# Optimization experiments

Measured on AMD Instinct MI355X. Metric: run time of the kernel, lower is better.

Reference implementation:

```python
import jax, jax.numpy as jnp
import numpy as np

DIM = 1024
DIM_HEAD = 64
HEADS = 16
DIM_INNER = DIM_HEAD * HEADS  # 1024


def setup_inputs() -> dict:
    key = jax.random.key(0)
    k1, k2, k3 = jax.random.split(key, 3)
    b, n = 2, 2048
    x = jax.random.normal(k1, (b, n, DIM), dtype=jnp.float32)
    gamma = jnp.ones((DIM,), dtype=jnp.float32)
    # torch Linear weight [out,in] applied as x @ W.T; store pre-transposed [in,out]
    w_qkv = jax.random.normal(k2, (DIM, 3 * DIM_INNER), dtype=jnp.float32) * (DIM ** -0.5)
    w_out = jax.random.normal(k3, (DIM_INNER, DIM), dtype=jnp.float32) * (DIM_INNER ** -0.5)
    return {"x": x, "gamma": gamma, "w_qkv": w_qkv, "w_out": w_out}


def reference(x, gamma, w_qkv, w_out):
    h, d = HEADS, DIM_HEAD
    scale = d ** -0.5
    rms_scale = DIM ** 0.5
    # RMSNorm: F.normalize(x, dim=-1) * sqrt(dim) * gamma  (eps=1e-12 clamp on L2 norm)
    norm = jnp.maximum(jnp.linalg.norm(x, axis=-1, keepdims=True), 1e-12)
    xn = x / norm * rms_scale * gamma
    b, n, _ = x.shape
    qkv = xn @ w_qkv  # [b, n, 3*h*d]
    qkv = qkv.reshape(b, n, 3, h, d)
    q = qkv[:, :, 0].transpose(0, 2, 1, 3) * scale  # [b, h, n, d]
    k = qkv[:, :, 1].transpose(0, 2, 1, 3)
    v = qkv[:, :, 2].transpose(0, 2, 1, 3)
    sim = jnp.einsum('bhid,bhjd->bhij', q, k)  # [b, h, n, n]
    causal_mask = jnp.triu(jnp.ones((n, n), dtype=bool), k=1)
    neg = -jnp.finfo(sim.dtype).max
    sim = jnp.where(causal_mask, neg, sim)
    attn = jax.nn.softmax(sim, axis=-1)
    out = jnp.einsum('bhij,bhjd->bhid', attn, v)  # [b, h, n, d]
    out = out.transpose(0, 2, 1, 3).reshape(b, n, h * d)
    return out @ w_out
```

## Files before the change

### kernel.cpp

```cpp
#include <hip/hip_runtime.h>
#include <hip/hip_bf16.h>

typedef __bf16 bf16x8 __attribute__((ext_vector_type(8)));
typedef short s16x4 __attribute__((ext_vector_type(4)));
typedef float f32x4 __attribute__((ext_vector_type(4)));
typedef unsigned short u16x8 __attribute__((ext_vector_type(8)));

#define MFMA_K32(a, b, c) __builtin_amdgcn_mfma_f32_16x16x32_bf16(a, b, c, 0, 0, 0)

static __device__ __forceinline__ f32x4 mfma_k16(s16x4 a, s16x4 b, f32x4 c) {
#ifdef __HIP_DEVICE_COMPILE__
    return __builtin_amdgcn_mfma_f32_16x16x16bf16_1k(a, b, c, 0, 0, 0);
#else
    return c;
#endif
}

static __device__ __forceinline__ float fast_exp2(float x) {
#ifdef __HIP_DEVICE_COMPILE__
    return __builtin_amdgcn_exp2f(x);
#else
    return x;
#endif
}

#define GLL16(gp, lp)                                              \
    __builtin_amdgcn_global_load_lds(                              \
        (const __attribute__((address_space(1))) void*)(gp),       \
        (__attribute__((address_space(3))) void*)(lp), 16, 0, 0)

static __device__ __forceinline__ unsigned short f2bf(float f) {
    unsigned int u = __float_as_uint(f);
    u += 0x7fffu + ((u >> 16) & 1u);
    return (unsigned short)(u >> 16);
}

static __device__ __forceinline__ unsigned int cvtpk_bf16(float lo, float hi) {
#if defined(__HIP_DEVICE_COMPILE__) && __has_builtin(__builtin_amdgcn_cvt_pk_bf16_f32)
    typedef __bf16 bf16x2 __attribute__((ext_vector_type(2)));
    bf16x2 r = __builtin_amdgcn_cvt_pk_bf16_f32(lo, hi);
    return __builtin_bit_cast(unsigned int, r);
#else
    return (unsigned int)f2bf(lo) | ((unsigned int)f2bf(hi) << 16);
#endif
}

#define LOG2E 1.44269504088896340736f

__global__ __launch_bounds__(256) void prep_k(
    const float* __restrict__ x, const float* __restrict__ gamma,
    const float* __restrict__ w_qkv, const float* __restrict__ w_out,
    unsigned short* __restrict__ xn, unsigned short* __restrict__ wtq,
    unsigned short* __restrict__ wto) {
    __shared__ float sm[32][33];
    int bid = blockIdx.x, tid = threadIdx.x;
    if (bid < 4096) {
        const float* in;
        unsigned short* out;
        int R = 1024, C, bx, by;
        if (bid < 3072) { in = w_qkv; out = wtq; C = 3072; bx = bid % 96; by = bid / 96; }
        else { int b2 = bid - 3072; in = w_out; out = wto; C = 1024; bx = b2 % 32; by = b2 / 32; }
        int c0 = bx * 32, r0 = by * 32;
        int tr = tid >> 5, tc = tid & 31;
#pragma unroll
        for (int i = 0; i < 4; i++)
            sm[tr + i * 8][tc] = in[(size_t)(r0 + tr + i * 8) * C + c0 + tc];
        __syncthreads();
#pragma unroll
        for (int i = 0; i < 4; i++)
            out[(size_t)(c0 + tr + i * 8) * R + r0 + tc] = f2bf(sm[tc][tr + i * 8]);
    } else {
        int row = bid - 4096;
        const float* xr = x + (size_t)row * 1024;
        float4 v = *(const float4*)(xr + tid * 4);
        float ss = v.x * v.x + v.y * v.y + v.z * v.z + v.w * v.w;
#pragma unroll
        for (int off = 1; off < 64; off <<= 1) ss += __shfl_xor(ss, off, 64);
        if ((tid & 63) == 0) sm[0][tid >> 6] = ss;
        __syncthreads();
        float tot = sm[0][0] + sm[0][1] + sm[0][2] + sm[0][3];
        float f = 32.0f / fmaxf(sqrtf(tot), 1e-12f);
        float4 g = *(const float4*)(gamma + tid * 4);
        uint2 o;
        o.x = cvtpk_bf16(v.x * f * g.x, v.y * f * g.y);
        o.y = cvtpk_bf16(v.z * f * g.z, v.w * f * g.w);
        *(uint2*)(xn + (size_t)row * 1024 + tid * 4) = o;
    }
}

template <int MODE, int BM>
__global__ __launch_bounds__(256) void gemm_bt_k(
    const unsigned short* __restrict__ A, const unsigned short* __restrict__ BT,
    float* __restrict__ C, unsigned short* __restrict__ qw,
    unsigned short* __restrict__ kw, unsigned short* __restrict__ vw,
    int M, int N, int K) {
    constexpr int RT = 4;
    constexpr int CT = (BM == 128) ? 4 : 2;
    __shared__ unsigned short As[BM][32];
    __shared__ unsigned short Bs[128][32];
    int tid = threadIdx.x;
    int wave = tid >> 6, lane = tid & 63, quad = lane >> 4, l16 = lane & 15;
    int wrb, wcb;
    if constexpr (BM == 128) { wrb = (wave >> 1) * 64; wcb = (wave & 1) * 64; }
    else { wrb = 0; wcb = wave * 32; }
    int m0 = blockIdx.y * BM, n0 = blockIdx.x * 128;
    int lrow = lane >> 2, lcol = (lane & 3) * 8;
    const unsigned short *Ag0, *Ag1 = nullptr;
    if constexpr (BM == 128) {
        Ag0 = A + (size_t)(m0 + wave * 32 + lrow) * K + lcol;
        Ag1 = A + (size_t)(m0 + wave * 32 + 16 + lrow) * K + lcol;
    } else {
        Ag0 = A + (size_t)(m0 + wave * 16 + lrow) * K + lcol;
    }
    const unsigned short* Bg0 = BT + (size_t)(n0 + wave * 32 + lrow) * K + lcol;
    const unsigned short* Bg1 = BT + (size_t)(n0 + wave * 32 + 16 + lrow) * K + lcol;
    f32x4 acc[RT][CT] = {};
    for (int k0 = 0; k0 < K; k0 += 32) {
        __syncthreads();
        if constexpr (BM == 128) {
            GLL16(Ag0 + k0, &As[wave * 32][0]);
            GLL16(Ag1 + k0, &As[wave * 32 + 16][0]);
        } else {
            GLL16(Ag0 + k0, &As[wave * 16][0]);
        }
        GLL16(Bg0 + k0, &Bs[wave * 32][0]);
        GLL16(Bg1 + k0, &Bs[wave * 32 + 16][0]);
        __syncthreads();
        bf16x8 af[RT], bfr[CT];
#pragma unroll
        for (int t = 0; t < RT; t++)
            af[t] = *(const bf16x8*)&As[wrb + t * 16 + l16][quad * 8];
#pragma unroll
        for (int t = 0; t < CT; t++)
            bfr[t] = *(const bf16x8*)&Bs[wcb + t * 16 + l16][quad * 8];
#pragma unroll
        for (int rt = 0; rt < RT; rt++)
#pragma unroll
            for (int ct = 0; ct < CT; ct++)
                acc[rt][ct] = MFMA_K32(af[rt], bfr[ct], acc[rt][ct]);
    }
#pragma unroll
    for (int rt = 0; rt < RT; rt++) {
        int mb = m0 + wrb + rt * 16 + quad * 4;
        int b = mb >> 11, nn = mb & 2047;
#pragma unroll
        for (int ct = 0; ct < CT; ct++) {
            int col = n0 + wcb + ct * 16 + l16;
            if (MODE == 0) {
#pragma unroll
                for (int r = 0; r < 4; r++)
                    C[(size_t)(mb + r) * N + col] = acc[rt][ct][r];
            } else {
                int sec = col >> 10, ci = col & 1023;
                int hh = ci >> 6, dd = ci & 63;
                int bh = b * 16 + hh;
                if (sec == 0) {
#pragma unroll
                    for (int r = 0; r < 4; r++)
                        qw[((size_t)bh * 2048 + nn + r) * 64 + dd] =
                            f2bf(acc[rt][ct][r] * (0.125f * LOG2E));
                } else if (sec == 1) {
#pragma unroll
                    for (int r = 0; r < 4; r++)
                        kw[((size_t)bh * 2048 + nn + r) * 64 + dd] = f2bf(acc[rt][ct][r]);
                } else {
                    uint2 pk;
                    pk.x = cvtpk_bf16(acc[rt][ct][0], acc[rt][ct][1]);
                    pk.y = cvtpk_bf16(acc[rt][ct][2], acc[rt][ct][3]);
                    *(uint2*)&vw[((size_t)bh * 64 + dd) * 2048 + nn] = pk;
                }
            }
        }
    }
}

__global__ __launch_bounds__(256) void attn_k(
    const unsigned short* __restrict__ q, const unsigned short* __restrict__ k,
    const unsigned short* __restrict__ vt, unsigned short* __restrict__ o) {
    __shared__ unsigned short Ks[2][64][72];
    __shared__ unsigned short Vt[2][64][72];
    int bh = blockIdx.x;
    int qt = 31 - (int)blockIdx.y;
    int tid = threadIdx.x, wave = tid >> 6, lane = tid & 63;
    int quad = lane >> 4, l16 = lane & 15;
    int b = bh >> 4, h = bh & 15;
    const unsigned short* qg = q + (size_t)bh * 2048 * 64;
    const unsigned short* kg = k + (size_t)bh * 2048 * 64;
    const unsigned short* vg = vt + (size_t)bh * 64 * 2048;
    int srow = tid >> 2, scol = (tid & 3) * 16;
    u16x8 pk0, pk1, pv0, pv1;
    int q0w = qt * 64 + wave * 16;
    bf16x8 bq[2];
#pragma unroll
    for (int ks = 0; ks < 2; ks++)
        bq[ks] = *(const bf16x8*)&qg[(size_t)(q0w + l16) * 64 + ks * 32 + quad * 8];
    f32x4 ot[4] = {};
    float mrun = -1e38f, lrun = 0.f;
    int nkt = qt + 1;
    {
        const unsigned short* kp = kg + (size_t)srow * 64 + scol;
        pk0 = *(const u16x8*)kp;
        pk1 = *(const u16x8*)(kp + 8);
        const unsigned short* vp = vg + (size_t)srow * 2048 + scol;
        pv0 = *(const u16x8*)vp;
        pv1 = *(const u16x8*)(vp + 8);
        *(u16x8*)&Ks[0][srow][scol] = pk0;
        *(u16x8*)&Ks[0][srow][scol + 8] = pk1;
        *(u16x8*)&Vt[0][srow][scol] = pv0;
        *(u16x8*)&Vt[0][srow][scol + 8] = pv1;
    }
    __syncthreads();
    for (int kt = 0; kt < nkt; kt++) {
        int cb = kt & 1;
        bool pf = (kt + 1 < nkt);
        if (pf) {
            const unsigned short* kp = kg + (size_t)((kt + 1) * 64 + srow) * 64 + scol;
            pk0 = *(const u16x8*)kp;
            pk1 = *(const u16x8*)(kp + 8);
            const unsigned short* vp = vg + (size_t)srow * 2048 + (kt + 1) * 64 + scol;
            pv0 = *(const u16x8*)vp;
            pv1 = *(const u16x8*)(vp + 8);
        }
        f32x4 sf[4];
#pragma unroll
        for (int ct = 0; ct < 4; ct++) {
            bf16x8 ak0 = *(const bf16x8*)&Ks[cb][ct * 16 + l16][quad * 8];
            bf16x8 ak1 = *(const bf16x8*)&Ks[cb][ct * 16 + l16][32 + quad * 8];
            f32x4 s = {};
            s = MFMA_K32(ak0, bq[0], s);
            s = MFMA_K32(ak1, bq[1], s);
            sf[ct] = s;
        }
        if (kt == qt) {
            int qloc = wave * 16 + l16;
#pragma unroll
            for (int ct = 0; ct < 4; ct++)
#pragma unroll
                for (int r = 0; r < 4; r++)
                    if (ct * 16 + quad * 4 + r > qloc) sf[ct][r] = -1e30f;
        }
        float mx = -1e30f;
#pragma unroll
        for (int ct = 0; ct < 4; ct++)
#pragma unroll
            for (int r = 0; r < 4; r++) mx = fmaxf(mx, sf[ct][r]);
        mx = fmaxf(mx, __shfl_xor(mx, 16, 64));
        mx = fmaxf(mx, __shfl_xor(mx, 32, 64));
        float mnew = fmaxf(mrun, mx);
        float al = fast_exp2(mrun - mnew);
        mrun = mnew;
        float rs = 0.f;
#pragma unroll
        for (int ct = 0; ct < 4; ct++)
#pragma unroll
            for (int r = 0; r < 4; r++) {
                float p = fast_exp2(sf[ct][r] - mnew);
                sf[ct][r] = p;
                rs += p;
            }
        rs += __shfl_xor(rs, 16, 64);
        rs += __shfl_xor(rs, 32, 64);
        lrun = lrun * al + rs;
        s16x4 bpr[4];
#pragma unroll
        for (int ct = 0; ct < 4; ct++) {
            uint2 u;
            u.x = cvtpk_bf16(sf[ct][0], sf[ct][1]);
            u.y = cvtpk_bf16(sf[ct][2], sf[ct][3]);
            bpr[ct] = __builtin_bit_cast(s16x4, u);
        }
#pragma unroll
        for (int dt = 0; dt < 4; dt++) {
#pragma unroll
            for (int r = 0; r < 4; r++) ot[dt][r] *= al;
#pragma unroll
            for (int ct = 0; ct < 4; ct++) {
                s16x4 av = *(const s16x4*)&Vt[cb][dt * 16 + l16][ct * 16 + quad * 4];
                ot[dt] = mfma_k16(av, bpr[ct], ot[dt]);
            }
        }
        if (pf) {
            *(u16x8*)&Ks[1 - cb][srow][scol] = pk0;
            *(u16x8*)&Ks[1 - cb][srow][scol + 8] = pk1;
            *(u16x8*)&Vt[1 - cb][srow][scol] = pv0;
            *(u16x8*)&Vt[1 - cb][srow][scol + 8] = pv1;
        }
        __syncthreads();
    }
    float inv = 1.0f / lrun;
    size_t rowbase = ((size_t)b * 2048 + q0w + l16) * 1024 + h * 64;
#pragma unroll
    for (int dt = 0; dt < 4; dt++) {
        uint2 pk;
        pk.x = cvtpk_bf16(ot[dt][0] * inv, ot[dt][1] * inv);
        pk.y = cvtpk_bf16(ot[dt][2] * inv, ot[dt][3] * inv);
        *(uint2*)&o[rowbase + dt * 16 + quad * 4] = pk;
    }
}

extern "C" void kernel_launch(void* const* d_in, const int* in_sizes, int n_in,
                              void* d_out, int out_size, void* d_ws, size_t ws_size,
                              hipStream_t stream) {
    const float* x = (const float*)d_in[0];
    const float* gamma = (const float*)d_in[1];
    const float* w_qkv = (const float*)d_in[2];
    const float* w_out = (const float*)d_in[3];
    float* out = (float*)d_out;
    char* ws = (char*)d_ws;

    unsigned short* xn = (unsigned short*)(ws);
    unsigned short* wtq = (unsigned short*)(ws + 8388608);
    unsigned short* wto = (unsigned short*)(ws + 14680064);
    unsigned short* qw = (unsigned short*)(ws + 16777216);
    unsigned short* kw = (unsigned short*)(ws + 25165824);
    unsigned short* vw = (unsigned short*)(ws + 33554432);
    unsigned short* ao = xn;

    prep_k<<<8192, 256, 0, stream>>>(x, gamma, w_qkv, w_out, xn, wtq, wto);
    gemm_bt_k<1, 128><<<dim3(24, 32), 256, 0, stream>>>(xn, wtq, nullptr, qw, kw, vw,
                                                        4096, 3072, 1024);
    attn_k<<<dim3(32, 32), 256, 0, stream>>>(qw, kw, vw, ao);
    gemm_bt_k<0, 64><<<dim3(8, 64), 256, 0, stream>>>(ao, wto, out, nullptr, nullptr,
                                                      nullptr, 4096, 1024, 1024);
}
```

Before: 190.8 us.

## Double attention key tile to 128 and permute V layout for wide LDS reads

The attention kernel now processes 128 keys per iteration instead of 64, which halves the number of loop iterations and barriers. The QKV GEMM epilogue writes V transposed with a permuted column order inside each 64-block, so one 8-wide LDS load supplies two k16 MFMA operands. It also skips the output rescale when no lane's running max changed. The costs are more LDS and registers per block and more wasted masked work on the last tile, since the diagonal tile now spans 128 keys.

```diff
diff --git a/kernel.cpp b/kernel.cpp
--- a/kernel.cpp
+++ b/kernel.cpp
@@ -3,6 +3,7 @@
 
 typedef __bf16 bf16x8 __attribute__((ext_vector_type(8)));
 typedef short s16x4 __attribute__((ext_vector_type(4)));
+typedef short s16x8 __attribute__((ext_vector_type(8)));
 typedef float f32x4 __attribute__((ext_vector_type(4)));
 typedef unsigned short u16x8 __attribute__((ext_vector_type(8)));
 
@@ -167,7 +168,8 @@
                     uint2 pk;
                     pk.x = cvtpk_bf16(acc[rt][ct][0], acc[rt][ct][1]);
                     pk.y = cvtpk_bf16(acc[rt][ct][2], acc[rt][ct][3]);
-                    *(uint2*)&vw[((size_t)bh * 64 + dd) * 2048 + nn] = pk;
+                    int sb = (nn & ~63) | (((nn >> 2) & 3) << 4) | (((nn >> 4) & 3) << 2);
+                    *(uint2*)&vw[((size_t)bh * 64 + dd) * 2048 + sb] = pk;
                 }
             }
         }
@@ -177,8 +179,8 @@
 __global__ __launch_bounds__(256) void attn_k(
     const unsigned short* __restrict__ q, const unsigned short* __restrict__ k,
     const unsigned short* __restrict__ vt, unsigned short* __restrict__ o) {
-    __shared__ unsigned short Ks[2][64][72];
-    __shared__ unsigned short Vt[2][64][72];
+    __shared__ unsigned short Ks[2][128][72];
+    __shared__ unsigned short Vt[2][64][136];
     int bh = blockIdx.x;
     int qt = 31 - (int)blockIdx.y;
     int tid = threadIdx.x, wave = tid >> 6, lane = tid & 63;
@@ -187,8 +189,8 @@
     const unsigned short* qg = q + (size_t)bh * 2048 * 64;
     const unsigned short* kg = k + (size_t)bh * 2048 * 64;
     const unsigned short* vg = vt + (size_t)bh * 64 * 2048;
-    int srow = tid >> 2, scol = (tid & 3) * 16;
-    u16x8 pk0, pk1, pv0, pv1;
+    int krow = tid >> 1, kcol = (tid & 1) * 32;
+    int vrow = tid >> 2, vcol = (tid & 3) * 32;
     int q0w = qt * 64 + wave * 16;
     bf16x8 bq[2];
 #pragma unroll
@@ -196,34 +198,38 @@
         bq[ks] = *(const bf16x8*)&qg[(size_t)(q0w + l16) * 64 + ks * 32 + quad * 8];
     f32x4 ot[4] = {};
     float mrun = -1e38f, lrun = 0.f;
-    int nkt = qt + 1;
+    int nkt = (qt >> 1) + 1;
+    u16x8 pk[4], pv[4];
     {
-        const unsigned short* kp = kg + (size_t)srow * 64 + scol;
-        pk0 = *(const u16x8*)kp;
-        pk1 = *(const u16x8*)(kp + 8);
-        const unsigned short* vp = vg + (size_t)srow * 2048 + scol;
-        pv0 = *(const u16x8*)vp;
-        pv1 = *(const u16x8*)(vp + 8);
-        *(u16x8*)&Ks[0][srow][scol] = pk0;
-        *(u16x8*)&Ks[0][srow][scol + 8] = pk1;
-        *(u16x8*)&Vt[0][srow][scol] = pv0;
-        *(u16x8*)&Vt[0][srow][scol + 8] = pv1;
+        const unsigned short* kp = kg + (size_t)krow * 64 + kcol;
+        const unsigned short* vp = vg + (size_t)vrow * 2048 + vcol;
+#pragma unroll
+        for (int i = 0; i < 4; i++) {
+            pk[i] = *(const u16x8*)(kp + i * 8);
+            pv[i] = *(const u16x8*)(vp + i * 8);
+        }
+#pragma unroll
+        for (int i = 0; i < 4; i++) {
+            *(u16x8*)&Ks[0][krow][kcol + i * 8] = pk[i];
+            *(u16x8*)&Vt[0][vrow][vcol + i * 8] = pv[i];
+        }
     }
     __syncthreads();
     for (int kt = 0; kt < nkt; kt++) {
         int cb = kt & 1;
         bool pf = (kt + 1 < nkt);
         if (pf) {
-            const unsigned short* kp = kg + (size_t)((kt + 1) * 64 + srow) * 64 + scol;
-            pk0 = *(const u16x8*)kp;
-            pk1 = *(const u16x8*)(kp + 8);
-            const unsigned short* vp = vg + (size_t)srow * 2048 + (kt + 1) * 64 + scol;
-            pv0 = *(const u16x8*)vp;
-            pv1 = *(const u16x8*)(vp + 8);
-        }
-        f32x4 sf[4];
-#pragma unroll
-        for (int ct = 0; ct < 4; ct++) {
+            const unsigned short* kp = kg + (size_t)((kt + 1) * 128 + krow) * 64 + kcol;
+            const unsigned short* vp = vg + (size_t)vrow * 2048 + (kt + 1) * 128 + vcol;
+#pragma unroll
+            for (int i = 0; i < 4; i++) {
+                pk[i] = *(const u16x8*)(kp + i * 8);
+                pv[i] = *(const u16x8*)(vp + i * 8);
+            }
+        }
+        f32x4 sf[8];
+#pragma unroll
+        for (int ct = 0; ct < 8; ct++) {
             bf16x8 ak0 = *(const bf16x8*)&Ks[cb][ct * 16 + l16][quad * 8];
             bf16x8 ak1 = *(const bf16x8*)&Ks[cb][ct * 16 + l16][32 + quad * 8];
             f32x4 s = {};
@@ -231,17 +237,18 @@
             s = MFMA_K32(ak1, bq[1], s);
             sf[ct] = s;
         }
-        if (kt == qt) {
-            int qloc = wave * 16 + l16;
-#pragma unroll
-            for (int ct = 0; ct < 4; ct++)
+        if (kt == nkt - 1) {
+            int qrow = q0w + l16;
+            int keyb = kt * 128 + quad * 4;
+#pragma unroll
+            for (int ct = 0; ct < 8; ct++)
 #pragma unroll
                 for (int r = 0; r < 4; r++)
-                    if (ct * 16 + quad * 4 + r > qloc) sf[ct][r] = -1e30f;
+                    if (keyb + ct * 16 + r > qrow) sf[ct][r] = -1e30f;
         }
         float mx = -1e30f;
 #pragma unroll
-        for (int ct = 0; ct < 4; ct++)
+        for (int ct = 0; ct < 8; ct++)
 #pragma unroll
             for (int r = 0; r < 4; r++) mx = fmaxf(mx, sf[ct][r]);
         mx = fmaxf(mx, __shfl_xor(mx, 16, 64));
@@ -251,7 +258,7 @@
         mrun = mnew;
         float rs = 0.f;
 #pragma unroll
-        for (int ct = 0; ct < 4; ct++)
+        for (int ct = 0; ct < 8; ct++)
 #pragma unroll
             for (int r = 0; r < 4; r++) {
                 float p = fast_exp2(sf[ct][r] - mnew);
@@ -261,29 +268,41 @@
         rs += __shfl_xor(rs, 16, 64);
         rs += __shfl_xor(rs, 32, 64);
         lrun = lrun * al + rs;
-        s16x4 bpr[4];
-#pragma unroll
-        for (int ct = 0; ct < 4; ct++) {
+        s16x4 bpr[8];
+#pragma unroll
+        for (int ct = 0; ct < 8; ct++) {
             uint2 u;
             u.x = cvtpk_bf16(sf[ct][0], sf[ct][1]);
             u.y = cvtpk_bf16(sf[ct][2], sf[ct][3]);
             bpr[ct] = __builtin_bit_cast(s16x4, u);
         }
+        if (__any(al < 1.0f)) {
+#pragma unroll
+            for (int dt = 0; dt < 4; dt++)
+#pragma unroll
+                for (int r = 0; r < 4; r++) ot[dt][r] *= al;
+        }
 #pragma unroll
         for (int dt = 0; dt < 4; dt++) {
 #pragma unroll
-            for (int r = 0; r < 4; r++) ot[dt][r] *= al;
-#pragma unroll
-            for (int ct = 0; ct < 4; ct++) {
-                s16x4 av = *(const s16x4*)&Vt[cb][dt * 16 + l16][ct * 16 + quad * 4];
-                ot[dt] = mfma_k16(av, bpr[ct], ot[dt]);
+            for (int blk = 0; blk < 2; blk++)
+#pragma unroll
+                for (int p = 0; p < 2; p++) {
+                    s16x8 av = *(const s16x8*)&Vt[cb][dt * 16 + l16]
+                                                  [blk * 64 + quad * 16 + p * 8];
+                    s16x4 lo = __builtin_shufflevector(av, av, 0, 1, 2, 3);
+                    s16x4 hi = __builtin_shufflevector(av, av, 4, 5, 6, 7);
+                    int ct = blk * 4 + p * 2;
+                    ot[dt] = mfma_k16(lo, bpr[ct], ot[dt]);
+                    ot[dt] = mfma_k16(hi, bpr[ct + 1], ot[dt]);
+                }
+        }
+        if (pf) {
+#pragma unroll
+            for (int i = 0; i < 4; i++) {
+                *(u16x8*)&Ks[1 - cb][krow][kcol + i * 8] = pk[i];
+                *(u16x8*)&Vt[1 - cb][vrow][vcol + i * 8] = pv[i];
             }
-        }
-        if (pf) {
-            *(u16x8*)&Ks[1 - cb][srow][scol] = pk0;
-            *(u16x8*)&Ks[1 - cb][srow][scol + 8] = pk1;
-            *(u16x8*)&Vt[1 - cb][srow][scol] = pv0;
-            *(u16x8*)&Vt[1 - cb][srow][scol + 8] = pv1;
         }
         __syncthreads();
     }
@@ -291,10 +310,10 @@
     size_t rowbase = ((size_t)b * 2048 + q0w + l16) * 1024 + h * 64;
 #pragma unroll
     for (int dt = 0; dt < 4; dt++) {
-        uint2 pk;
-        pk.x = cvtpk_bf16(ot[dt][0] * inv, ot[dt][1] * inv);
-        pk.y = cvtpk_bf16(ot[dt][2] * inv, ot[dt][3] * inv);
-        *(uint2*)&o[rowbase + dt * 16 + quad * 4] = pk;
+        uint2 pk2;
+        pk2.x = cvtpk_bf16(ot[dt][0] * inv, ot[dt][1] * inv);
+        pk2.y = cvtpk_bf16(ot[dt][2] * inv, ot[dt][3] * inv);
+        *(uint2*)&o[rowbase + dt * 16 + quad * 4] = pk2;
     }
 }
 
```

Result: no change. 191.8 us (+0.5%).
